# Kernel optimization log

Measured on AMD Instinct MI355X. Metric: run time of the kernel, lower is better.

## Reference

```python
import jax, jax.numpy as jnp
import numpy as np

B, S, I, H = 64, 512, 512, 512


def setup_inputs() -> dict:
    key = jax.random.key(0)
    ks = jax.random.split(key, 5)
    scale = 1.0 / np.sqrt(I + H)  # keep gates out of hard saturation
    return {
        "x": jax.random.normal(ks[0], (B, S, I), dtype=jnp.float32),
        "h": jax.random.normal(ks[1], (B, H), dtype=jnp.float32),
        "W_r": jax.random.normal(ks[2], (H, I + H), dtype=jnp.float32) * scale,
        "b_r": jnp.zeros((H,), dtype=jnp.float32),
        "W_z": jax.random.normal(ks[3], (H, I + H), dtype=jnp.float32) * scale,
        "b_z": jnp.zeros((H,), dtype=jnp.float32),
        "W_h": jax.random.normal(ks[4], (H, I + H), dtype=jnp.float32) * scale,
        "b_h": jnp.zeros((H,), dtype=jnp.float32),
    }


def reference(x, h, W_r, b_r, W_z, b_z, W_h, b_h):
    # Split each [H, I+H] weight into input part and hidden part (torch cat order: [x, h]).
    i = x.shape[-1]
    Wr_x, Wr_h = W_r[:, :i], W_r[:, i:]
    Wz_x, Wz_h = W_z[:, :i], W_z[:, i:]
    Wh_x, Wh_h = W_h[:, :i], W_h[:, i:]

    # Precompute the input contributions for all timesteps in one big GEMM each.
    xr = jnp.einsum("bsi,hi->bsh", x, Wr_x) + b_r  # [B,S,H]
    xz = jnp.einsum("bsi,hi->bsh", x, Wz_x) + b_z
    xh = jnp.einsum("bsi,hi->bsh", x, Wh_x) + b_h

    def step(h, inp):
        xr_t, xz_t, xh_t = inp  # each [B,H]
        r = jax.nn.sigmoid(xr_t + h @ Wr_h.T)
        z = jax.nn.sigmoid(xz_t + h @ Wz_h.T)
        h_tilde = jnp.tanh(xh_t + (r * h) @ Wh_h.T)
        h_new = (1.0 - z) * h + z * h_tilde
        return h_new, h_new

    # time-major for scan
    xs = (xr.transpose(1, 0, 2), xz.transpose(1, 0, 2), xh.transpose(1, 0, 2))
    h_last, ys = jax.lax.scan(step, h, xs)
    y = ys.transpose(1, 0, 2)  # [B,S,H]; dropout p=0 -> identity
    return y, h_last
```

## Files before the change

### kernel.cpp

```cpp
#include <hip/hip_runtime.h>

#define B_ 64
#define S_ 512
#define H_ 512

typedef unsigned short u16;
typedef unsigned int   u32;
typedef unsigned long long u64;

typedef __attribute__((ext_vector_type(8))) short    bf16x8;
typedef __attribute__((ext_vector_type(8))) _Float16 f16x8;
typedef __attribute__((ext_vector_type(4))) float    f32x4;
typedef __attribute__((ext_vector_type(2))) _Float16 h2_t;

#define PJ_GATE ((size_t)512 * 64 * 512)

__device__ inline u16 f2bf(float f) {
  u32 u = __builtin_bit_cast(u32, f);
  u32 r = (u + 0x7fffu + ((u >> 16) & 1u)) >> 16;
  return (u16)r;
}
__device__ inline u32 pkbf2(float a, float b) {
  return (u32)f2bf(a) | ((u32)f2bf(b) << 16);
}
__device__ inline u16 f2h(float a) {
  _Float16 x = (_Float16)a;
  return __builtin_bit_cast(u16, x);
}
__device__ inline u32 pk2h(float a, float b) {
  return (u32)f2h(a) | ((u32)f2h(b) << 16);
}
__device__ inline float sigmoidf_(float x) { return 1.f / (1.f + __expf(-x)); }
__device__ inline float tanhf_(float x) {
  float e = __expf(-2.f * fabsf(x));
  float t = (1.f - e) / (1.f + e);
  return copysignf(t, x);
}
__device__ inline void xstore(u32* p, u32 v) {
  __hip_atomic_store(p, v, __ATOMIC_RELAXED, __HIP_MEMORY_SCOPE_AGENT);
}
__device__ inline u64 xload(const u64* p) {
  return __hip_atomic_load(p, __ATOMIC_RELAXED, __HIP_MEMORY_SCOPE_AGENT);
}

__global__ void k_convert_w(const float* __restrict__ Wr, const float* __restrict__ Wz,
                            const float* __restrict__ Wh, uint4* __restrict__ WF) {
  int g = blockIdx.y;
  const float* Ws = (g == 0) ? Wr : ((g == 1) ? Wz : Wh);
  int i = blockIdx.x * 256 + threadIdx.x;
  int lane = i & 63;
  int kt   = (i >> 6) & 15;
  int rt   = i >> 10;
  int row  = rt * 16 + (lane & 15);
  int col  = 512 + kt * 32 + (lane >> 4) * 8;
  const float* src = Ws + (size_t)row * 1024 + col;
  float4 a = *(const float4*)src;
  float4 b = *(const float4*)(src + 4);
  uint4 o;
  o.x = pk2h(a.x, a.y); o.y = pk2h(a.z, a.w);
  o.z = pk2h(b.x, b.y); o.w = pk2h(b.z, b.w);
  WF[((size_t)(g * 32 + rt) * 16 + kt) * 64 + lane] = o;
}

__global__ __launch_bounds__(256) void k_proj_gemm(
    const float* __restrict__ x,
    const float* __restrict__ Wr, const float* __restrict__ Wz, const float* __restrict__ Wh,
    const float* __restrict__ br, const float* __restrict__ bz, const float* __restrict__ bh,
    u16* __restrict__ P)
{
  const int g  = blockIdx.z;
  const int bm = blockIdx.x * 64;
  const int bn = blockIdx.y * 64;
  const float* Ws = (g == 0) ? Wr : ((g == 1) ? Wz : Wh);
  __shared__ __align__(16) u16 As[64][32];
  __shared__ __align__(16) u16 Bs[64][32];
  const int tid  = threadIdx.x;
  const int lane = tid & 63;
  const int wm   = (tid >> 6) >> 1;
  const int wn   = (tid >> 6) & 1;
  const int srow = tid >> 2;
  const int scol = (tid & 3) * 8;

  f32x4 zero4 = {0.f, 0.f, 0.f, 0.f};
  f32x4 acc[2][2];
  acc[0][0] = zero4; acc[0][1] = zero4; acc[1][0] = zero4; acc[1][1] = zero4;

  for (int k0 = 0; k0 < 512; k0 += 32) {
    __syncthreads();
    {
      const float* xs = x + (size_t)(bm + srow) * 512 + k0 + scol;
      float4 a = *(const float4*)xs, b = *(const float4*)(xs + 4);
      uint4 av; av.x = pkbf2(a.x, a.y); av.y = pkbf2(a.z, a.w);
      av.z = pkbf2(b.x, b.y); av.w = pkbf2(b.z, b.w);
      *(uint4*)(&As[srow][scol]) = av;
      const float* wsrc = Ws + (size_t)(bn + srow) * 1024 + k0 + scol;
      float4 c = *(const float4*)wsrc, d = *(const float4*)(wsrc + 4);
      uint4 bv; bv.x = pkbf2(c.x, c.y); bv.y = pkbf2(c.z, c.w);
      bv.z = pkbf2(d.x, d.y); bv.w = pkbf2(d.z, d.w);
      *(uint4*)(&Bs[srow][scol]) = bv;
    }
    __syncthreads();
#pragma unroll
    for (int mi = 0; mi < 2; ++mi) {
      bf16x8 a = *(const bf16x8*)(&As[wm * 32 + mi * 16 + (lane & 15)][(lane >> 4) * 8]);
#pragma unroll
      for (int ni = 0; ni < 2; ++ni) {
        bf16x8 b = *(const bf16x8*)(&Bs[wn * 32 + ni * 16 + (lane & 15)][(lane >> 4) * 8]);
        acc[mi][ni] = __builtin_amdgcn_mfma_f32_16x16x32_bf16(a, b, acc[mi][ni], 0, 0, 0);
      }
    }
  }
  const float* bias = (g == 0) ? br : ((g == 1) ? bz : bh);
#pragma unroll
  for (int mi = 0; mi < 2; ++mi)
#pragma unroll
    for (int ni = 0; ni < 2; ++ni) {
      int col  = bn + wn * 32 + ni * 16 + (lane & 15);
      float bv = bias[col];
#pragma unroll
      for (int r = 0; r < 4; ++r) {
        int row = bm + wm * 32 + mi * 16 + (lane >> 4) * 4 + r;
        int bb = row >> 9, ss = row & 511;
        float v = acc[mi][ni][r] + bv;
        P[((size_t)g * 512 + ss) * (64 * 512) + (size_t)bb * 512 + col] =
            __builtin_bit_cast(u16, (_Float16)v);
      }
    }
}

__global__ __launch_bounds__(512, 2) void k_gru_scan(
    const float* __restrict__ h0,
    const u16*  __restrict__ P,
    const uint4* __restrict__ WF,
    u32* __restrict__ RHX,
    u32* __restrict__ HX,
    float* __restrict__ y,
    float* __restrict__ hlast)
{
  const int q = blockIdx.x & 3;
  const int c = blockIdx.x >> 2;
  const int t = threadIdx.x;
  const int w = t >> 6;
  const int l = t & 63;
  const int bq = l & 15;
  const int g4 = l >> 4;
  const int bglob = c * 16 + bq;
  const int rt  = q * 8 + w;
  const int j0A = q * 128 + w * 16 + g4 * 4;

  __shared__ __align__(16) u16 hbuf[16 * 520];
  __shared__ __align__(16) u16 rhbuf[16 * 520];

  f16x8 wr[16], wz[16], wh[16];
#pragma unroll
  for (int kt = 0; kt < 16; ++kt) {
    wr[kt] = __builtin_bit_cast(f16x8, WF[((size_t)(0 * 32 + rt) * 16 + kt) * 64 + l]);
    wz[kt] = __builtin_bit_cast(f16x8, WF[((size_t)(1 * 32 + rt) * 16 + kt) * 64 + l]);
    wh[kt] = __builtin_bit_cast(f16x8, WF[((size_t)(2 * 32 + rt) * 16 + kt) * 64 + l]);
  }

  f32x4 hold = *(const f32x4*)(h0 + (size_t)bglob * 512 + j0A);
  {
    int b = t >> 5, j = (t & 31) * 16;
    const float4* s = (const float4*)(h0 + (size_t)(c * 16 + b) * 512 + j);
    float4 v0 = s[0], v1 = s[1], v2 = s[2], v3 = s[3];
    uint4 o0, o1;
    o0.x = pk2h(v0.x, v0.y); o0.y = pk2h(v0.z, v0.w);
    o0.z = pk2h(v1.x, v1.y); o0.w = pk2h(v1.z, v1.w);
    o1.x = pk2h(v2.x, v2.y); o1.y = pk2h(v2.z, v2.w);
    o1.z = pk2h(v3.x, v3.y); o1.w = pk2h(v3.z, v3.w);
    uint4* d = (uint4*)&hbuf[b * 520 + j];
    d[0] = o0; d[1] = o1;
  }
  __syncthreads();

  const u16* Ppr = P + (size_t)bglob * 512 + j0A;
  const u16* Ppz = P + PJ_GATE + (size_t)bglob * 512 + j0A;
  const u16* Pph = P + 2 * PJ_GATE + (size_t)bglob * 512 + j0A;

  const int kL = t >> 2;
  const int b0 = (t & 3) * 4;
  const int CL = 512 * 16;
  const int PAR = 4 * CL;

  uint2 pru = *(const uint2*)Ppr;
  uint2 pzu = *(const uint2*)Ppz;

  for (int ts = 0; ts < S_; ++ts) {
    const int par = ts & 1;
    const u32 tag = (u32)(ts + 1);
    const u64 tp  = ((u64)tag << 16) | ((u64)tag << 48);
    u32* RHXp = RHX + par * PAR + c * CL;
    u32* HXp  = HX  + par * PAR + c * CL;

    uint2 phu = *(const uint2*)(Pph + (size_t)ts * 32768);

    f32x4 ar = {0.f, 0.f, 0.f, 0.f}, az = {0.f, 0.f, 0.f, 0.f};
#pragma unroll
    for (int kt = 0; kt < 16; ++kt) {
      f16x8 hv = *(const f16x8*)&hbuf[bq * 520 + g4 * 8 + kt * 32];
      ar = __builtin_amdgcn_mfma_f32_16x16x32_f16(wr[kt], hv, ar, 0, 0, 0);
      az = __builtin_amdgcn_mfma_f32_16x16x32_f16(wz[kt], hv, az, 0, 0, 0);
    }
    h2_t pr0 = __builtin_bit_cast(h2_t, pru.x), pr1 = __builtin_bit_cast(h2_t, pru.y);
    h2_t pz0 = __builtin_bit_cast(h2_t, pzu.x), pz1 = __builtin_bit_cast(h2_t, pzu.y);
    float rr0 = sigmoidf_(ar[0] + (float)pr0[0]);
    float rr1 = sigmoidf_(ar[1] + (float)pr0[1]);
    float rr2 = sigmoidf_(ar[2] + (float)pr1[0]);
    float rr3 = sigmoidf_(ar[3] + (float)pr1[1]);
    float zz0 = sigmoidf_(az[0] + (float)pz0[0]);
    float zz1 = sigmoidf_(az[1] + (float)pz0[1]);
    float zz2 = sigmoidf_(az[2] + (float)pz1[0]);
    float zz3 = sigmoidf_(az[3] + (float)pz1[1]);
    u16 rh0 = f2h(rr0 * hold[0]), rh1 = f2h(rr1 * hold[1]);
    u16 rh2 = f2h(rr2 * hold[2]), rh3 = f2h(rr3 * hold[3]);
    *(uint2*)&rhbuf[bq * 520 + j0A] =
        uint2{(u32)rh0 | ((u32)rh1 << 16), (u32)rh2 | ((u32)rh3 << 16)};
    xstore(RHXp + (j0A + 0) * 16 + bq, (tag << 16) | rh0);
    xstore(RHXp + (j0A + 1) * 16 + bq, (tag << 16) | rh1);
    xstore(RHXp + (j0A + 2) * 16 + bq, (tag << 16) | rh2);
    xstore(RHXp + (j0A + 3) * 16 + bq, (tag << 16) | rh3);

#pragma unroll
    for (int p = 1; p < 4; ++p) {
      int pq = (q + p) & 3;
      int kg = pq * 128 + kL;
      const u64* pa = (const u64*)(RHXp + kg * 16 + b0);
      u64 A = xload(pa), Bv = xload(pa + 1);
      while (((A ^ tp) & 0xffff0000ffff0000ull) != 0ull) {
        __builtin_amdgcn_s_sleep(1);
        A = xload(pa);
      }
      while (((Bv ^ tp) & 0xffff0000ffff0000ull) != 0ull) {
        __builtin_amdgcn_s_sleep(1);
        Bv = xload(pa + 1);
      }
      rhbuf[(b0 + 0) * 520 + kg] = (u16)A;
      rhbuf[(b0 + 1) * 520 + kg] = (u16)(A >> 32);
      rhbuf[(b0 + 2) * 520 + kg] = (u16)Bv;
      rhbuf[(b0 + 3) * 520 + kg] = (u16)(Bv >> 32);
    }
    __syncthreads();

    f32x4 ah = {0.f, 0.f, 0.f, 0.f};
#pragma unroll
    for (int kt = 0; kt < 16; ++kt) {
      f16x8 rv = *(const f16x8*)&rhbuf[bq * 520 + g4 * 8 + kt * 32];
      ah = __builtin_amdgcn_mfma_f32_16x16x32_f16(wh[kt], rv, ah, 0, 0, 0);
    }
    h2_t ph0 = __builtin_bit_cast(h2_t, phu.x), ph1 = __builtin_bit_cast(h2_t, phu.y);
    float ht0 = tanhf_(ah[0] + (float)ph0[0]);
    float ht1 = tanhf_(ah[1] + (float)ph0[1]);
    float ht2 = tanhf_(ah[2] + (float)ph1[0]);
    float ht3 = tanhf_(ah[3] + (float)ph1[1]);
    f32x4 hn;
    hn[0] = zz0 * ht0 + (1.f - zz0) * hold[0];
    hn[1] = zz1 * ht1 + (1.f - zz1) * hold[1];
    hn[2] = zz2 * ht2 + (1.f - zz2) * hold[2];
    hn[3] = zz3 * ht3 + (1.f - zz3) * hold[3];
    hold = hn;
    __builtin_nontemporal_store(hn,
        (f32x4*)(y + (size_t)bglob * 262144 + (size_t)ts * 512 + j0A));
    u16 h0b = f2h(hn[0]), h1b = f2h(hn[1]), h2b = f2h(hn[2]), h3b = f2h(hn[3]);
    *(uint2*)&hbuf[bq * 520 + j0A] =
        uint2{(u32)h0b | ((u32)h1b << 16), (u32)h2b | ((u32)h3b << 16)};
    xstore(HXp + (j0A + 0) * 16 + bq, (tag << 16) | h0b);
    xstore(HXp + (j0A + 1) * 16 + bq, (tag << 16) | h1b);
    xstore(HXp + (j0A + 2) * 16 + bq, (tag << 16) | h2b);
    xstore(HXp + (j0A + 3) * 16 + bq, (tag << 16) | h3b);

    {
      int tsn = (ts < S_ - 1) ? ts + 1 : ts;
      pru = *(const uint2*)(Ppr + (size_t)tsn * 32768);
      pzu = *(const uint2*)(Ppz + (size_t)tsn * 32768);
    }

#pragma unroll
    for (int p = 1; p < 4; ++p) {
      int pq = (q + p) & 3;
      int jg = pq * 128 + kL;
      const u64* pa = (const u64*)(HXp + jg * 16 + b0);
      u64 A = xload(pa), Bv = xload(pa + 1);
      while (((A ^ tp) & 0xffff0000ffff0000ull) != 0ull) {
        __builtin_amdgcn_s_sleep(1);
        A = xload(pa);
      }
      while (((Bv ^ tp) & 0xffff0000ffff0000ull) != 0ull) {
        __builtin_amdgcn_s_sleep(1);
        Bv = xload(pa + 1);
      }
      hbuf[(b0 + 0) * 520 + jg] = (u16)A;
      hbuf[(b0 + 1) * 520 + jg] = (u16)(A >> 32);
      hbuf[(b0 + 2) * 520 + jg] = (u16)Bv;
      hbuf[(b0 + 3) * 520 + jg] = (u16)(Bv >> 32);
    }
    __syncthreads();
  }

  *(f32x4*)(hlast + (size_t)bglob * 512 + j0A) = hold;
}

extern "C" void kernel_launch(void* const* d_in, const int* in_sizes, int n_in,
                              void* d_out, int out_size, void* d_ws, size_t ws_size,
                              hipStream_t stream) {
  const float* x  = (const float*)d_in[0];
  const float* h0 = (const float*)d_in[1];
  const float* Wr = (const float*)d_in[2];
  const float* br = (const float*)d_in[3];
  const float* Wz = (const float*)d_in[4];
  const float* bz = (const float*)d_in[5];
  const float* Wh = (const float*)d_in[6];
  const float* bh = (const float*)d_in[7];

  char* ws = (char*)d_ws;
  uint4* WF  = (uint4*)ws;
  u16*   P   = (u16*)(ws + 2097152);
  u32*   RHX = (u32*)(ws + 102760448);
  u32*   HX  = (u32*)(ws + 103022592);

  float* y     = (float*)d_out;
  float* hlast = y + (size_t)B_ * S_ * H_;

  hipMemsetAsync(ws + 102760448, 0, 524288, stream);
  k_convert_w<<<dim3(128, 3), dim3(256), 0, stream>>>(Wr, Wz, Wh, WF);
  k_proj_gemm<<<dim3(512, 8, 3), dim3(256), 0, stream>>>(x, Wr, Wz, Wh, br, bz, bh, P);
  k_gru_scan<<<dim3(16), dim3(512), 0, stream>>>(h0, P, WF, RHX, HX, y, hlast);
}
```

Before: 3.188 ms.

## Move Wh weights to LDS, batch-major exchange layout with 64-bit stores, share hbuf

Moves the W_h hidden-weight fragments out of registers into a 128 KB LDS buffer, cutting register pressure. The cross-block exchange buffers switch from feature-major to batch-major layout, so each thread publishes four tagged values with two 64-bit atomic stores and polls contiguous 64-bit words, writing packed uint2 into LDS instead of scattered u16 writes. The separate rhbuf is dropped and hbuf is reused for r*h, which needs an extra __syncthreads per phase. The trade-off is LDS reads of W_h inside the MFMA loop, lower occupancy from the large LDS allocation, and two additional barriers per timestep.

Result: slower. 3.552 ms (+11.4%).

```diff
diff --git a/kernel.cpp b/kernel.cpp
--- a/kernel.cpp
+++ b/kernel.cpp
@@ -36,7 +36,7 @@
   float t = (1.f - e) / (1.f + e);
   return copysignf(t, x);
 }
-__device__ inline void xstore(u32* p, u32 v) {
+__device__ inline void xstore64(u64* p, u64 v) {
   __hip_atomic_store(p, v, __ATOMIC_RELAXED, __HIP_MEMORY_SCOPE_AGENT);
 }
 __device__ inline u64 xload(const u64* p) {
@@ -148,16 +148,20 @@
   const int rt  = q * 8 + w;
   const int j0A = q * 128 + w * 16 + g4 * 4;
 
+  __shared__ __align__(16) u16 whlds[8 * 16 * 512];
   __shared__ __align__(16) u16 hbuf[16 * 520];
-  __shared__ __align__(16) u16 rhbuf[16 * 520];
-
-  f16x8 wr[16], wz[16], wh[16];
+
+  f16x8 wr[16], wz[16];
 #pragma unroll
   for (int kt = 0; kt < 16; ++kt) {
     wr[kt] = __builtin_bit_cast(f16x8, WF[((size_t)(0 * 32 + rt) * 16 + kt) * 64 + l]);
     wz[kt] = __builtin_bit_cast(f16x8, WF[((size_t)(1 * 32 + rt) * 16 + kt) * 64 + l]);
-    wh[kt] = __builtin_bit_cast(f16x8, WF[((size_t)(2 * 32 + rt) * 16 + kt) * 64 + l]);
-  }
+    *(uint4*)&whlds[((w * 16 + kt) * 64 + l) * 8] =
+        WF[((size_t)(2 * 32 + rt) * 16 + kt) * 64 + l];
+  }
+#pragma unroll
+  for (int kt = 0; kt < 16; ++kt)
+    asm volatile("" : "+v"(wr[kt]), "+v"(wz[kt]));
 
   f32x4 hold = *(const f32x4*)(h0 + (size_t)bglob * 512 + j0A);
   {
@@ -178,13 +182,44 @@
   const u16* Ppz = P + PJ_GATE + (size_t)bglob * 512 + j0A;
   const u16* Pph = P + 2 * PJ_GATE + (size_t)bglob * 512 + j0A;
 
-  const int kL = t >> 2;
-  const int b0 = (t & 3) * 4;
-  const int CL = 512 * 16;
+  const int bR = t >> 5;
+  const int kR = (t & 31) * 4;
+  const int k1 = ((q + 1) & 3) * 128 + kR;
+  const int k2 = ((q + 2) & 3) * 128 + kR;
+  const int k3 = ((q + 3) & 3) * 128 + kR;
+  const int CL  = 16 * 512;
   const int PAR = 4 * CL;
 
   uint2 pru = *(const uint2*)Ppr;
   uint2 pzu = *(const uint2*)Ppz;
+
+#define POLL_INTO_HBUF(Xp)                                                      \
+  {                                                                             \
+    const u64* p1 = (const u64*)((Xp) + bR * 512 + k1);                         \
+    const u64* p2 = (const u64*)((Xp) + bR * 512 + k2);                         \
+    const u64* p3 = (const u64*)((Xp) + bR * 512 + k3);                         \
+    u64 A1 = xload(p1), B1 = xload(p1 + 1);                                     \
+    u64 A2 = xload(p2), B2 = xload(p2 + 1);                                     \
+    u64 A3 = xload(p3), B3 = xload(p3 + 1);                                     \
+    while (((A1 ^ tp) & TMASK) != 0ull) { __builtin_amdgcn_s_sleep(1); A1 = xload(p1); } \
+    while (((B1 ^ tp) & TMASK) != 0ull) { __builtin_amdgcn_s_sleep(1); B1 = xload(p1 + 1); } \
+    while (((A2 ^ tp) & TMASK) != 0ull) { __builtin_amdgcn_s_sleep(1); A2 = xload(p2); } \
+    while (((B2 ^ tp) & TMASK) != 0ull) { __builtin_amdgcn_s_sleep(1); B2 = xload(p2 + 1); } \
+    while (((A3 ^ tp) & TMASK) != 0ull) { __builtin_amdgcn_s_sleep(1); A3 = xload(p3); } \
+    while (((B3 ^ tp) & TMASK) != 0ull) { __builtin_amdgcn_s_sleep(1); B3 = xload(p3 + 1); } \
+    uint2 w1, w2, w3;                                                           \
+    w1.x = (u32)(A1 & 0xffffu) | (((u32)(A1 >> 32) & 0xffffu) << 16);           \
+    w1.y = (u32)(B1 & 0xffffu) | (((u32)(B1 >> 32) & 0xffffu) << 16);           \
+    w2.x = (u32)(A2 & 0xffffu) | (((u32)(A2 >> 32) & 0xffffu) << 16);           \
+    w2.y = (u32)(B2 & 0xffffu) | (((u32)(B2 >> 32) & 0xffffu) << 16);           \
+    w3.x = (u32)(A3 & 0xffffu) | (((u32)(A3 >> 32) & 0xffffu) << 16);           \
+    w3.y = (u32)(B3 & 0xffffu) | (((u32)(B3 >> 32) & 0xffffu) << 16);           \
+    *(uint2*)&hbuf[bR * 520 + k1] = w1;                                         \
+    *(uint2*)&hbuf[bR * 520 + k2] = w2;                                         \
+    *(uint2*)&hbuf[bR * 520 + k3] = w3;                                         \
+  }
+
+  const u64 TMASK = 0xffff0000ffff0000ull;
 
   for (int ts = 0; ts < S_; ++ts) {
     const int par = ts & 1;
@@ -214,39 +249,24 @@
     float zz3 = sigmoidf_(az[3] + (float)pz1[1]);
     u16 rh0 = f2h(rr0 * hold[0]), rh1 = f2h(rr1 * hold[1]);
     u16 rh2 = f2h(rr2 * hold[2]), rh3 = f2h(rr3 * hold[3]);
-    *(uint2*)&rhbuf[bq * 520 + j0A] =
+    {
+      u64 v01 = (u64)((tag << 16) | rh0) | ((u64)((tag << 16) | rh1) << 32);
+      u64 v23 = (u64)((tag << 16) | rh2) | ((u64)((tag << 16) | rh3) << 32);
+      xstore64((u64*)(RHXp + bq * 512 + j0A), v01);
+      xstore64((u64*)(RHXp + bq * 512 + j0A + 2), v23);
+    }
+    __syncthreads();
+    *(uint2*)&hbuf[bq * 520 + j0A] =
         uint2{(u32)rh0 | ((u32)rh1 << 16), (u32)rh2 | ((u32)rh3 << 16)};
-    xstore(RHXp + (j0A + 0) * 16 + bq, (tag << 16) | rh0);
-    xstore(RHXp + (j0A + 1) * 16 + bq, (tag << 16) | rh1);
-    xstore(RHXp + (j0A + 2) * 16 + bq, (tag << 16) | rh2);
-    xstore(RHXp + (j0A + 3) * 16 + bq, (tag << 16) | rh3);
-
-#pragma unroll
-    for (int p = 1; p < 4; ++p) {
-      int pq = (q + p) & 3;
-      int kg = pq * 128 + kL;
-      const u64* pa = (const u64*)(RHXp + kg * 16 + b0);
-      u64 A = xload(pa), Bv = xload(pa + 1);
-      while (((A ^ tp) & 0xffff0000ffff0000ull) != 0ull) {
-        __builtin_amdgcn_s_sleep(1);
-        A = xload(pa);
-      }
-      while (((Bv ^ tp) & 0xffff0000ffff0000ull) != 0ull) {
-        __builtin_amdgcn_s_sleep(1);
-        Bv = xload(pa + 1);
-      }
-      rhbuf[(b0 + 0) * 520 + kg] = (u16)A;
-      rhbuf[(b0 + 1) * 520 + kg] = (u16)(A >> 32);
-      rhbuf[(b0 + 2) * 520 + kg] = (u16)Bv;
-      rhbuf[(b0 + 3) * 520 + kg] = (u16)(Bv >> 32);
-    }
+    POLL_INTO_HBUF(RHXp)
     __syncthreads();
 
     f32x4 ah = {0.f, 0.f, 0.f, 0.f};
 #pragma unroll
     for (int kt = 0; kt < 16; ++kt) {
-      f16x8 rv = *(const f16x8*)&rhbuf[bq * 520 + g4 * 8 + kt * 32];
-      ah = __builtin_amdgcn_mfma_f32_16x16x32_f16(wh[kt], rv, ah, 0, 0, 0);
+      f16x8 rv = *(const f16x8*)&hbuf[bq * 520 + g4 * 8 + kt * 32];
+      f16x8 wh = *(const f16x8*)&whlds[((w * 16 + kt) * 64 + l) * 8];
+      ah = __builtin_amdgcn_mfma_f32_16x16x32_f16(wh, rv, ah, 0, 0, 0);
     }
     h2_t ph0 = __builtin_bit_cast(h2_t, phu.x), ph1 = __builtin_bit_cast(h2_t, phu.y);
     float ht0 = tanhf_(ah[0] + (float)ph0[0]);
@@ -262,12 +282,12 @@
     __builtin_nontemporal_store(hn,
         (f32x4*)(y + (size_t)bglob * 262144 + (size_t)ts * 512 + j0A));
     u16 h0b = f2h(hn[0]), h1b = f2h(hn[1]), h2b = f2h(hn[2]), h3b = f2h(hn[3]);
-    *(uint2*)&hbuf[bq * 520 + j0A] =
-        uint2{(u32)h0b | ((u32)h1b << 16), (u32)h2b | ((u32)h3b << 16)};
-    xstore(HXp + (j0A + 0) * 16 + bq, (tag << 16) | h0b);
-    xstore(HXp + (j0A + 1) * 16 + bq, (tag << 16) | h1b);
-    xstore(HXp + (j0A + 2) * 16 + bq, (tag << 16) | h2b);
-    xstore(HXp + (j0A + 3) * 16 + bq, (tag << 16) | h3b);
+    {
+      u64 v01 = (u64)((tag << 16) | h0b) | ((u64)((tag << 16) | h1b) << 32);
+      u64 v23 = (u64)((tag << 16) | h2b) | ((u64)((tag << 16) | h3b) << 32);
+      xstore64((u64*)(HXp + bq * 512 + j0A), v01);
+      xstore64((u64*)(HXp + bq * 512 + j0A + 2), v23);
+    }
 
     {
       int tsn = (ts < S_ - 1) ? ts + 1 : ts;
@@ -275,25 +295,10 @@
       pzu = *(const uint2*)(Ppz + (size_t)tsn * 32768);
     }
 
-#pragma unroll
-    for (int p = 1; p < 4; ++p) {
-      int pq = (q + p) & 3;
-      int jg = pq * 128 + kL;
-      const u64* pa = (const u64*)(HXp + jg * 16 + b0);
-      u64 A = xload(pa), Bv = xload(pa + 1);
-      while (((A ^ tp) & 0xffff0000ffff0000ull) != 0ull) {
-        __builtin_amdgcn_s_sleep(1);
-        A = xload(pa);
-      }
-      while (((Bv ^ tp) & 0xffff0000ffff0000ull) != 0ull) {
-        __builtin_amdgcn_s_sleep(1);
-        Bv = xload(pa + 1);
-      }
-      hbuf[(b0 + 0) * 520 + jg] = (u16)A;
-      hbuf[(b0 + 1) * 520 + jg] = (u16)(A >> 32);
-      hbuf[(b0 + 2) * 520 + jg] = (u16)Bv;
-      hbuf[(b0 + 3) * 520 + jg] = (u16)(Bv >> 32);
-    }
+    __syncthreads();
+    *(uint2*)&hbuf[bq * 520 + j0A] =
+        uint2{(u32)h0b | ((u32)h1b << 16), (u32)h2b | ((u32)h3b << 16)};
+    POLL_INTO_HBUF(HXp)
     __syncthreads();
   }
 
```
